# Kernel optimization log

Measured on AMD Instinct MI355X. Metric: run time of the kernel, lower is better.

## Reference

```python
import jax, jax.numpy as jnp
import numpy as np

B, S, D, H = 4, 2048, 1024, 16
DH = D // H
NEG = -10000.0


def setup_inputs() -> dict:
    key = jax.random.key(0)
    ks = jax.random.split(key, 12)
    scale = 0.02
    inp = {
        "q": jax.random.normal(ks[0], (B, S, D), jnp.float32),
        "k": jax.random.normal(ks[1], (B, S, D), jnp.float32),
        "v": jax.random.normal(ks[2], (B, S, D), jnp.float32),
        "mask": jnp.triu(jnp.ones((S, S), jnp.bool_), k=1),  # True = masked (causal)
        "Wq": jax.random.normal(ks[3], (D, D), jnp.float32) * scale,
        "bq": jnp.zeros((D,), jnp.float32),
        "Wk": jax.random.normal(ks[4], (D, D), jnp.float32) * scale,
        "bk": jnp.zeros((D,), jnp.float32),
        "Wv": jax.random.normal(ks[5], (D, D), jnp.float32) * scale,
        "bv": jnp.zeros((D,), jnp.float32),
        "Wo": jax.random.normal(ks[6], (D, D), jnp.float32) * scale,
        "bo": jnp.zeros((D,), jnp.float32),
    }
    return inp


def _split(x):
    # [B,S,D] -> [B,H,S,DH]
    return x.reshape(B, S, H, DH).transpose(0, 2, 1, 3)


def reference(q, k, v, mask, Wq, bq, Wk, bk, Wv, bv, Wo, bo):
    # torch Linear: y = x @ W.T + b
    qh = _split(q @ Wq.T + bq)
    kh = _split(k @ Wk.T + bk)
    vh = _split(v @ Wv.T + bv)
    # scaled dot-product scores: [B,H,S,S]
    scores = jnp.einsum("bhqd,bhkd->bhqk", qh, kh) / jnp.sqrt(jnp.float32(DH))
    scores = scores + jnp.where(mask, jnp.float32(NEG), jnp.float32(0.0))
    attn = jax.nn.softmax(scores, axis=-1)  # dropout_rate=0 -> identity
    out = jnp.einsum("bhqk,bhkd->bhqd", attn, vh)
    out = out.transpose(0, 2, 1, 3).reshape(B, S, D)
    return out @ Wo.T + bo
```

## Files before the change

kernel.cpp:

```cpp
#include <hip/hip_runtime.h>
#include <hip/hip_bf16.h>


#define B_ 4
#define S_ 2048
#define D_ 1024
#define H_ 16
#define DH_ 64
#define M_ (B_*S_)
#define MASKADD (-14427.0f)
#define QSCALE  (0.180336880f)

typedef __attribute__((ext_vector_type(8)))  __bf16 bf16x8;
typedef __attribute__((ext_vector_type(8)))  unsigned short ushort8;
typedef __attribute__((ext_vector_type(4)))  float f32x4;
typedef __attribute__((ext_vector_type(16))) float f32x16;

__device__ __forceinline__ unsigned short f2bf(float f) {
  __hip_bfloat16 h = __float2bfloat16(f);
  union { __hip_bfloat16 h; unsigned short u; } c; c.h = h; return c.u;
}

__device__ __forceinline__ f32x4 mfma16(bf16x8 a, bf16x8 b, f32x4 c) {
  return __builtin_amdgcn_mfma_f32_16x16x32_bf16(a, b, c, 0, 0, 0);
}
__device__ __forceinline__ f32x16 mfma32(bf16x8 a, bf16x8 b, f32x16 c) {
  return __builtin_amdgcn_mfma_f32_32x32x16_bf16(a, b, c, 0, 0, 0);
}

__device__ __forceinline__ unsigned cvtpk(float lo, float hi) {
  unsigned r;
  asm("v_cvt_pk_bf16_f32 %0, %1, %2" : "=v"(r) : "v"(lo), "v"(hi));
  return r;
}

__device__ __forceinline__ void gld_lds16(const void* g, void* l) {
  __builtin_amdgcn_global_load_lds(
      (const __attribute__((address_space(1))) unsigned int*)g,
      (__attribute__((address_space(3))) unsigned int*)l, 16, 0, 0);
}

__global__ void cvt4_kernel(const float* __restrict__ p0, const float* __restrict__ p1,
                            const float* __restrict__ p2, const float* __restrict__ p3,
                            unsigned short* __restrict__ o0, unsigned short* __restrict__ o1,
                            unsigned short* __restrict__ o2, unsigned short* __restrict__ o3,
                            int n4) {
  int i = blockIdx.x * blockDim.x + threadIdx.x;
  if (i >= n4) return;
  const float* in  = (blockIdx.y == 0) ? p0 : (blockIdx.y == 1 ? p1 : (blockIdx.y == 2 ? p2 : p3));
  unsigned short* out = (blockIdx.y == 0) ? o0 : (blockIdx.y == 1 ? o1 : (blockIdx.y == 2 ? o2 : o3));
  float4 f = reinterpret_cast<const float4*>(in)[i];
  ushort4 o;
  o.x = f2bf(f.x); o.y = f2bf(f.y); o.z = f2bf(f.z); o.w = f2bf(f.w);
  reinterpret_cast<ushort4*>(out)[i] = o;
}

template<bool F32A>
__device__ __forceinline__
void gemm_body(const void* __restrict__ Ap, const unsigned short* __restrict__ W,
               const float* __restrict__ bias, void* __restrict__ outp,
               int mode, bool sc,
               unsigned short* sA16, float* sA32, unsigned short* sB)
{
  const int tid  = threadIdx.x;
  const int lane = tid & 63, wid = tid >> 6;
  const int bx = blockIdx.x;
  const int j8 = bx & 7, i8 = bx >> 3;
  const int mt = j8*8 + (i8 >> 3), nt = i8 & 7;
  const int m0 = mt*128, n0 = nt*128;
  const int wr = wid >> 1, wc = wid & 1;
  const int g = lane >> 4;

  const float* A32 = (const float*)Ap;
  const unsigned short* A16 = (const unsigned short*)Ap;

  f32x4 acc[4][4];
  #pragma unroll
  for (int i = 0; i < 4; ++i)
    #pragma unroll
    for (int j = 0; j < 4; ++j)
      #pragma unroll
      for (int r = 0; r < 4; ++r) acc[i][j][r] = 0.0f;

  auto stageB = [&](int bufi, int kt) {
    const unsigned short* Wb = W + (size_t)n0*D_ + kt*32;
    #pragma unroll
    for (int p = 0; p < 2; ++p) {
      int r = 32*wid + 16*p + (lane >> 2);
      int c = (lane & 3) * 8;
      gld_lds16(Wb + (size_t)r*D_ + c, &sB[bufi*4096 + (32*wid + 16*p)*32]);
    }
  };
  auto stageA16 = [&](int bufi, int kt) {
    const unsigned short* Ab = A16 + (size_t)m0*D_ + kt*32;
    #pragma unroll
    for (int p = 0; p < 2; ++p) {
      int r = 32*wid + 16*p + (lane >> 2);
      int c = (lane & 3) * 8;
      gld_lds16(Ab + (size_t)r*D_ + c, &sA16[bufi*4096 + (32*wid + 16*p)*32]);
    }
  };
  auto stageA32 = [&](int bufi, int kt) {
    const float* Ab = A32 + (size_t)m0*D_ + kt*32;
    #pragma unroll
    for (int p = 0; p < 4; ++p) {
      int ch = 4*wid + p;
      int row = ch*8 + (lane >> 3);
      int cbs = ((lane & 7) * 16) ^ ((lane >> 3) << 4);
      gld_lds16(Ab + (size_t)row*D_ + (cbs >> 2), &sA32[bufi*4096 + ch*256]);
    }
  };

  if (F32A) stageA32(0, 0); else stageA16(0, 0);
  stageB(0, 0);

  const int NK = D_/32;
  int buf = 0;
  for (int kt = 0; kt < NK; ++kt) {
    __syncthreads();
    if (kt + 1 < NK) {
      if (F32A) stageA32(buf ^ 1, kt + 1);
      else      stageA16(buf ^ 1, kt + 1);
      stageB(buf ^ 1, kt + 1);
    }

    bf16x8 aF[4], bF[4];
    #pragma unroll
    for (int i = 0; i < 4; ++i) {
      int row = 64*wr + 16*i + (lane & 15);
      if (F32A) {
        const char* base = (const char*)(sA32 + buf*4096) + row*128;
        int sw = (row & 7) << 4;
        f32x4 a0 = *(const f32x4*)(base + ((g*32)      ^ sw));
        f32x4 a1 = *(const f32x4*)(base + ((g*32 + 16) ^ sw));
        union { unsigned u[4]; bf16x8 v; } af;
        af.u[0] = cvtpk(a0[0], a0[1]);
        af.u[1] = cvtpk(a0[2], a0[3]);
        af.u[2] = cvtpk(a1[0], a1[1]);
        af.u[3] = cvtpk(a1[2], a1[3]);
        aF[i] = af.v;
      } else {
        aF[i] = *(const bf16x8*)&sA16[buf*4096 + row*32 + g*8];
      }
    }
    #pragma unroll
    for (int j = 0; j < 4; ++j)
      bF[j] = *(const bf16x8*)&sB[buf*4096 + (64*wc + 16*j + (lane & 15))*32 + g*8];

    #pragma unroll
    for (int i = 0; i < 4; ++i)
      #pragma unroll
      for (int j = 0; j < 4; ++j)
        acc[i][j] = mfma16(aF[i], bF[j], acc[i][j]);
    buf ^= 1;
  }

  #pragma unroll
  for (int i = 0; i < 4; ++i) {
    int gr0 = m0 + 64*wr + 16*i + ((lane >> 4) << 2);
    #pragma unroll
    for (int j = 0; j < 4; ++j) {
      int gc = n0 + 64*wc + 16*j + (lane & 15);
      float bv = bias[gc];
      if (mode == 2) {
        int b = gr0 >> 11, s = gr0 & (S_ - 1);
        int hh = gc >> 6, dh = gc & (DH_ - 1);
        ushort4 o;
        o.x = f2bf(acc[i][j][0] + bv); o.y = f2bf(acc[i][j][1] + bv);
        o.z = f2bf(acc[i][j][2] + bv); o.w = f2bf(acc[i][j][3] + bv);
        *(ushort4*)&((unsigned short*)outp)[(((size_t)b*H_ + hh)*DH_ + dh)*S_ + s] = o;
      } else {
        #pragma unroll
        for (int r = 0; r < 4; ++r) {
          float v = acc[i][j][r] + bv;
          if (sc) v *= QSCALE;
          int gr = gr0 + r;
          if (mode == 0) {
            int b = gr >> 11, s = gr & (S_ - 1);
            int hh = gc >> 6, dh = gc & (DH_ - 1);
            ((unsigned short*)outp)[(((size_t)b*H_ + hh)*S_ + s)*DH_ + dh] = f2bf(v);
          } else {
            ((float*)outp)[(size_t)gr*D_ + gc] = v;
          }
        }
      }
    }
  }
}

__global__ __launch_bounds__(256, 3)
void gemm_qkv(const float* __restrict__ Aq, const float* __restrict__ Ak,
              const float* __restrict__ Av,
              const unsigned short* __restrict__ Wq_, const unsigned short* __restrict__ Wk_,
              const unsigned short* __restrict__ Wv_,
              const float* __restrict__ bq_, const float* __restrict__ bk_,
              const float* __restrict__ bv_,
              unsigned short* __restrict__ Oq, unsigned short* __restrict__ Ok,
              unsigned short* __restrict__ Ov)
{
  __shared__ float          sA32[2*4096];
  __shared__ unsigned short sB  [2*4096];
  const int y = blockIdx.y;
  const float* A = (y == 0) ? Aq : (y == 1 ? Ak : Av);
  const unsigned short* W = (y == 0) ? Wq_ : (y == 1 ? Wk_ : Wv_);
  const float* bias        = (y == 0) ? bq_ : (y == 1 ? bk_ : bv_);
  unsigned short* outp     = (y == 0) ? Oq  : (y == 1 ? Ok  : Ov);
  gemm_body<true>(A, W, bias, outp, (y == 2) ? 2 : 0, y == 0, nullptr, sA32, sB);
}

__global__ __launch_bounds__(256, 3)
void gemm_out(const unsigned short* __restrict__ A, const unsigned short* __restrict__ W,
              const float* __restrict__ bias, float* __restrict__ outp)
{
  __shared__ unsigned short sA16[2*4096];
  __shared__ unsigned short sB  [2*4096];
  gemm_body<false>(A, W, bias, outp, 1, false, sA16, nullptr, sB);
}

__global__ __launch_bounds__(256)
void attn_kernel(const unsigned short* __restrict__ Qh, const unsigned short* __restrict__ Kh,
                 const unsigned short* __restrict__ Vt, unsigned short* __restrict__ AO)
{
  __shared__ unsigned short sK [2][64*64];
  __shared__ unsigned short sVt[2][64*64];

  const int tid = threadIdx.x, lane = tid & 63, wid = tid >> 6;
  const int l31 = lane & 31, h5 = lane >> 5;
  const int bh = blockIdx.x;
  const int chunk = 15 - (int)blockIdx.y;
  const int bb = bh >> 4, hd = bh & 15;
  const unsigned short* Qb = Qh + (size_t)bh * S_ * DH_;
  const unsigned short* Kb = Kh + (size_t)bh * S_ * DH_;
  const unsigned short* Vb = Vt + (size_t)bh * DH_ * S_;
  const int qc0 = chunk * 128;
  const int NT  = 2*chunk + 2;
  const int qw0 = qc0 + wid*32;
  const int q   = qw0 + l31;

  bf16x8 qF[4];
  #pragma unroll
  for (int c = 0; c < 4; ++c)
    qF[c] = *(const bf16x8*)(Qb + (size_t)q*DH_ + c*16 + h5*8);

  f32x16 zz;
  #pragma unroll
  for (int r = 0; r < 16; ++r) zz[r] = 0.0f;
  f32x16 accO0 = zz, accO1 = zz;
  float lsum = 0.0f;

  auto stageK = [&](int bufi, int t) {
    #pragma unroll
    for (int p = 0; p < 2; ++p) {
      int ch = 2*wid + p;
      int row = ch*8 + (lane >> 3);
      int cbs = ((lane & 7) * 16) ^ ((row & 7) << 4);
      gld_lds16(Kb + (size_t)(t*64 + row)*DH_ + (cbs >> 1), &sK[bufi][ch*512]);
    }
  };
  auto stageV = [&](int bufi, int t) {
    #pragma unroll
    for (int p = 0; p < 2; ++p) {
      int ch = 2*wid + p;
      int row = ch*8 + (lane >> 3);
      int cbs = ((lane & 7) * 16) ^ ((row & 7) << 4);
      gld_lds16(Vb + (size_t)row*S_ + t*64 + (cbs >> 1), &sVt[bufi][ch*512]);
    }
  };

  stageK(0, 0);
  stageV(0, 0);

  int buf = 0;
  for (int t = 0; t < NT; ++t) {
    __syncthreads();
    if (t + 1 < NT) { stageK(buf ^ 1, t + 1); stageV(buf ^ 1, t + 1); }

    #pragma unroll
    for (int sub = 0; sub < 2; ++sub) {
      const int kv0 = t*64 + sub*32;
      if (kv0 > qw0 + 31) continue;
      const bool dodiag = (kv0 + 31 > qw0);

      f32x16 st = zz;
      __builtin_amdgcn_s_setprio(1);
      #pragma unroll
      for (int c = 0; c < 4; ++c) {
        int row = sub*32 + l31;
        const char* base = (const char*)&sK[buf][0] + row*128;
        bf16x8 kf = *(const bf16x8*)(base + ((32*c + 16*h5) ^ ((row & 7) << 4)));
        st = mfma32(kf, qF[c], st);
      }
      __builtin_amdgcn_s_setprio(0);

      #pragma unroll
      for (int r = 0; r < 16; ++r) {
        float x = st[r];
        if (dodiag) {
          int kv = kv0 + (r & 3) + 8*(r >> 2) + 4*h5;
          if (kv > q) x += MASKADD;
        }
        x = __builtin_amdgcn_exp2f(x);
        st[r] = x;
        lsum += x;
      }

      #pragma unroll
      for (int hh = 0; hh < 2; ++hh) {
        union { unsigned u[4]; bf16x8 v; } pb;
        pb.u[0] = cvtpk(st[8*hh+0], st[8*hh+1]);
        pb.u[1] = cvtpk(st[8*hh+2], st[8*hh+3]);
        pb.u[2] = cvtpk(st[8*hh+4], st[8*hh+5]);
        pb.u[3] = cvtpk(st[8*hh+6], st[8*hh+7]);

        __builtin_amdgcn_s_setprio(1);
        #pragma unroll
        for (int dh = 0; dh < 2; ++dh) {
          int row = dh*32 + l31;
          const char* base = (const char*)&sVt[buf][0] + row*128;
          int sw = (row & 7) << 4;
          int X = 64*sub + 32*hh + 8*h5;
          union { uint2 g[2]; bf16x8 v; } vv;
          vv.g[0] = *(const uint2*)(base + ((X)      ^ sw));
          vv.g[1] = *(const uint2*)(base + ((X + 16) ^ sw));
          if (dh == 0) accO0 = mfma32(vv.v, pb.v, accO0);
          else         accO1 = mfma32(vv.v, pb.v, accO1);
        }
        __builtin_amdgcn_s_setprio(0);
      }
    }
    buf ^= 1;
  }

  float lt = lsum + __shfl_xor(lsum, 32, 64);
  float inv = 1.0f / lt;
  unsigned short* ao = AO + ((size_t)bb*S_ + q)*D_ + hd*DH_;
  #pragma unroll
  for (int dh = 0; dh < 2; ++dh) {
    const f32x16 A = dh ? accO1 : accO0;
    #pragma unroll
    for (int rq = 0; rq < 4; ++rq) {
      ushort4 o;
      o.x = f2bf(A[4*rq+0] * inv);
      o.y = f2bf(A[4*rq+1] * inv);
      o.z = f2bf(A[4*rq+2] * inv);
      o.w = f2bf(A[4*rq+3] * inv);
      int dbase = dh*32 + 8*rq + 4*h5;
      *(ushort4*)&ao[dbase] = o;
    }
  }
}

extern "C" void kernel_launch(void* const* d_in, const int* in_sizes, int n_in,
                              void* d_out, int out_size, void* d_ws, size_t ws_size,
                              hipStream_t stream)
{
  const float* q  = (const float*)d_in[0];
  const float* k  = (const float*)d_in[1];
  const float* v  = (const float*)d_in[2];
  const float* Wq = (const float*)d_in[4];
  const float* bq = (const float*)d_in[5];
  const float* Wk = (const float*)d_in[6];
  const float* bk = (const float*)d_in[7];
  const float* Wv = (const float*)d_in[8];
  const float* bv = (const float*)d_in[9];
  const float* Wo = (const float*)d_in[10];
  const float* bo = (const float*)d_in[11];

  unsigned short* ws = (unsigned short*)d_ws;
  const size_t MD = (size_t)M_ * D_;
  const size_t DD = (size_t)D_ * D_;
  unsigned short* Wqb = ws;
  unsigned short* Wkb = Wqb + DD;
  unsigned short* Wvb = Wkb + DD;
  unsigned short* Wob = Wvb + DD;
  unsigned short* Qhb = Wob + DD;
  unsigned short* Khb = Qhb + MD;
  unsigned short* Vtb = Khb + MD;
  unsigned short* AOb = Vtb + MD;

  cvt4_kernel<<<dim3((int)(DD/4/256), 4), 256, 0, stream>>>(Wq, Wk, Wv, Wo, Wqb, Wkb, Wvb, Wob, (int)(DD/4));

  gemm_qkv<<<dim3(512, 3), 256, 0, stream>>>(q, k, v, Wqb, Wkb, Wvb,
                                             bq, bk, bv, Qhb, Khb, Vtb);

  attn_kernel<<<dim3(64, 16), 256, 0, stream>>>(Qhb, Khb, Vtb, AOb);

  gemm_out<<<512, 256, 0, stream>>>(AOb, Wob, bo, (float*)d_out);
}
```

Measured before the change: 175.8 us.

## Load fp32 activations directly to registers in QKV GEMM, bypassing LDS

The QKV projection GEMM no longer stages fp32 A tiles through shared memory. Each lane now loads its A fragment straight from global memory into registers, double-buffered across two register sets, and converts to bf16 just before the MFMA, while B stays staged in LDS. This removes the LDS traffic and the swizzled reads for A and cuts shared-memory use, at the cost of more registers (the occupancy hint of 3 is dropped) and less coalesced global reads of A. The out-projection GEMM is specialised inline and the shared epilogue is split into a helper.

```diff
diff --git a/kernel.cpp b/kernel.cpp
--- a/kernel.cpp
+++ b/kernel.cpp
@@ -55,106 +55,11 @@
   reinterpret_cast<ushort4*>(out)[i] = o;
 }
 
-template<bool F32A>
 __device__ __forceinline__
-void gemm_body(const void* __restrict__ Ap, const unsigned short* __restrict__ W,
-               const float* __restrict__ bias, void* __restrict__ outp,
-               int mode, bool sc,
-               unsigned short* sA16, float* sA32, unsigned short* sB)
+void gemm_epilogue(f32x4 (&acc)[4][4], const float* __restrict__ bias,
+                   void* __restrict__ outp, int mode, bool sc,
+                   int m0, int n0, int wr, int wc, int lane)
 {
-  const int tid  = threadIdx.x;
-  const int lane = tid & 63, wid = tid >> 6;
-  const int bx = blockIdx.x;
-  const int j8 = bx & 7, i8 = bx >> 3;
-  const int mt = j8*8 + (i8 >> 3), nt = i8 & 7;
-  const int m0 = mt*128, n0 = nt*128;
-  const int wr = wid >> 1, wc = wid & 1;
-  const int g = lane >> 4;
-
-  const float* A32 = (const float*)Ap;
-  const unsigned short* A16 = (const unsigned short*)Ap;
-
-  f32x4 acc[4][4];
-  #pragma unroll
-  for (int i = 0; i < 4; ++i)
-    #pragma unroll
-    for (int j = 0; j < 4; ++j)
-      #pragma unroll
-      for (int r = 0; r < 4; ++r) acc[i][j][r] = 0.0f;
-
-  auto stageB = [&](int bufi, int kt) {
-    const unsigned short* Wb = W + (size_t)n0*D_ + kt*32;
-    #pragma unroll
-    for (int p = 0; p < 2; ++p) {
-      int r = 32*wid + 16*p + (lane >> 2);
-      int c = (lane & 3) * 8;
-      gld_lds16(Wb + (size_t)r*D_ + c, &sB[bufi*4096 + (32*wid + 16*p)*32]);
-    }
-  };
-  auto stageA16 = [&](int bufi, int kt) {
-    const unsigned short* Ab = A16 + (size_t)m0*D_ + kt*32;
-    #pragma unroll
-    for (int p = 0; p < 2; ++p) {
-      int r = 32*wid + 16*p + (lane >> 2);
-      int c = (lane & 3) * 8;
-      gld_lds16(Ab + (size_t)r*D_ + c, &sA16[bufi*4096 + (32*wid + 16*p)*32]);
-    }
-  };
-  auto stageA32 = [&](int bufi, int kt) {
-    const float* Ab = A32 + (size_t)m0*D_ + kt*32;
-    #pragma unroll
-    for (int p = 0; p < 4; ++p) {
-      int ch = 4*wid + p;
-      int row = ch*8 + (lane >> 3);
-      int cbs = ((lane & 7) * 16) ^ ((lane >> 3) << 4);
-      gld_lds16(Ab + (size_t)row*D_ + (cbs >> 2), &sA32[bufi*4096 + ch*256]);
-    }
-  };
-
-  if (F32A) stageA32(0, 0); else stageA16(0, 0);
-  stageB(0, 0);
-
-  const int NK = D_/32;
-  int buf = 0;
-  for (int kt = 0; kt < NK; ++kt) {
-    __syncthreads();
-    if (kt + 1 < NK) {
-      if (F32A) stageA32(buf ^ 1, kt + 1);
-      else      stageA16(buf ^ 1, kt + 1);
-      stageB(buf ^ 1, kt + 1);
-    }
-
-    bf16x8 aF[4], bF[4];
-    #pragma unroll
-    for (int i = 0; i < 4; ++i) {
-      int row = 64*wr + 16*i + (lane & 15);
-      if (F32A) {
-        const char* base = (const char*)(sA32 + buf*4096) + row*128;
-        int sw = (row & 7) << 4;
-        f32x4 a0 = *(const f32x4*)(base + ((g*32)      ^ sw));
-        f32x4 a1 = *(const f32x4*)(base + ((g*32 + 16) ^ sw));
-        union { unsigned u[4]; bf16x8 v; } af;
-        af.u[0] = cvtpk(a0[0], a0[1]);
-        af.u[1] = cvtpk(a0[2], a0[3]);
-        af.u[2] = cvtpk(a1[0], a1[1]);
-        af.u[3] = cvtpk(a1[2], a1[3]);
-        aF[i] = af.v;
-      } else {
-        aF[i] = *(const bf16x8*)&sA16[buf*4096 + row*32 + g*8];
-      }
-    }
-    #pragma unroll
-    for (int j = 0; j < 4; ++j)
-      bF[j] = *(const bf16x8*)&sB[buf*4096 + (64*wc + 16*j + (lane & 15))*32 + g*8];
-
-    #pragma unroll
-    for (int i = 0; i < 4; ++i)
-      #pragma unroll
-      for (int j = 0; j < 4; ++j)
-        acc[i][j] = mfma16(aF[i], bF[j], acc[i][j]);
-    buf ^= 1;
-  }
-
   #pragma unroll
   for (int i = 0; i < 4; ++i) {
     int gr0 = m0 + 64*wr + 16*i + ((lane >> 4) << 2);
@@ -188,7 +93,7 @@
   }
 }
 
-__global__ __launch_bounds__(256, 3)
+__global__ __launch_bounds__(256)
 void gemm_qkv(const float* __restrict__ Aq, const float* __restrict__ Ak,
               const float* __restrict__ Av,
               const unsigned short* __restrict__ Wq_, const unsigned short* __restrict__ Wk_,
@@ -198,23 +103,158 @@
               unsigned short* __restrict__ Oq, unsigned short* __restrict__ Ok,
               unsigned short* __restrict__ Ov)
 {
-  __shared__ float          sA32[2*4096];
-  __shared__ unsigned short sB  [2*4096];
+  __shared__ unsigned short sB[2*4096];
   const int y = blockIdx.y;
   const float* A = (y == 0) ? Aq : (y == 1 ? Ak : Av);
   const unsigned short* W = (y == 0) ? Wq_ : (y == 1 ? Wk_ : Wv_);
   const float* bias        = (y == 0) ? bq_ : (y == 1 ? bk_ : bv_);
   unsigned short* outp     = (y == 0) ? Oq  : (y == 1 ? Ok  : Ov);
-  gemm_body<true>(A, W, bias, outp, (y == 2) ? 2 : 0, y == 0, nullptr, sA32, sB);
+  const int mode = (y == 2) ? 2 : 0;
+  const bool sc = (y == 0);
+
+  const int tid  = threadIdx.x;
+  const int lane = tid & 63, wid = tid >> 6;
+  const int bx = blockIdx.x;
+  const int j8 = bx & 7, i8 = bx >> 3;
+  const int mt = j8*8 + (i8 >> 3), nt = i8 & 7;
+  const int m0 = mt*128, n0 = nt*128;
+  const int wr = wid >> 1, wc = wid & 1;
+  const int g = lane >> 4;
+
+  f32x4 acc[4][4];
+  #pragma unroll
+  for (int i = 0; i < 4; ++i)
+    #pragma unroll
+    for (int j = 0; j < 4; ++j)
+      #pragma unroll
+      for (int r = 0; r < 4; ++r) acc[i][j][r] = 0.0f;
+
+  auto stageB = [&](int bufi, int kt) {
+    const unsigned short* Wb = W + (size_t)n0*D_ + kt*32;
+    #pragma unroll
+    for (int p = 0; p < 2; ++p) {
+      int r = 32*wid + 16*p + (lane >> 2);
+      int c = (lane & 3) * 8;
+      gld_lds16(Wb + (size_t)r*D_ + c, &sB[bufi*4096 + (32*wid + 16*p)*32]);
+    }
+  };
+
+  const float* arow[4];
+  #pragma unroll
+  for (int i = 0; i < 4; ++i)
+    arow[i] = A + (size_t)(m0 + 64*wr + 16*i + (lane & 15))*D_ + g*8;
+
+  f32x4 aR0[4][2], aR1[4][2];
+  auto loadA = [&](int kt, f32x4 (*aR)[2]) {
+    #pragma unroll
+    for (int i = 0; i < 4; ++i) {
+      const float* p = arow[i] + kt*32;
+      aR[i][0] = *(const f32x4*)(p);
+      aR[i][1] = *(const f32x4*)(p + 4);
+    }
+  };
+  auto mfmaStep = [&](const f32x4 (*aR)[2], int bufi) {
+    bf16x8 aF[4], bF[4];
+    #pragma unroll
+    for (int i = 0; i < 4; ++i) {
+      union { unsigned u[4]; bf16x8 v; } af;
+      af.u[0] = cvtpk(aR[i][0][0], aR[i][0][1]);
+      af.u[1] = cvtpk(aR[i][0][2], aR[i][0][3]);
+      af.u[2] = cvtpk(aR[i][1][0], aR[i][1][1]);
+      af.u[3] = cvtpk(aR[i][1][2], aR[i][1][3]);
+      aF[i] = af.v;
+    }
+    #pragma unroll
+    for (int j = 0; j < 4; ++j)
+      bF[j] = *(const bf16x8*)&sB[bufi*4096 + (64*wc + 16*j + (lane & 15))*32 + g*8];
+    #pragma unroll
+    for (int i = 0; i < 4; ++i)
+      #pragma unroll
+      for (int j = 0; j < 4; ++j)
+        acc[i][j] = mfma16(aF[i], bF[j], acc[i][j]);
+  };
+
+  loadA(0, aR0);
+  stageB(0, 0);
+
+  const int NK = D_/32;
+  for (int it = 0; it < NK/2; ++it) {
+    const int kt0 = 2*it;
+
+    __syncthreads();
+    stageB(1, kt0 + 1);
+    loadA(kt0 + 1, aR1);
+    mfmaStep(aR0, 0);
+
+    __syncthreads();
+    if (kt0 + 2 < NK) {
+      stageB(0, kt0 + 2);
+      loadA(kt0 + 2, aR0);
+    }
+    mfmaStep(aR1, 1);
+  }
+
+  gemm_epilogue(acc, bias, outp, mode, sc, m0, n0, wr, wc, lane);
 }
 
 __global__ __launch_bounds__(256, 3)
 void gemm_out(const unsigned short* __restrict__ A, const unsigned short* __restrict__ W,
               const float* __restrict__ bias, float* __restrict__ outp)
 {
-  __shared__ unsigned short sA16[2*4096];
-  __shared__ unsigned short sB  [2*4096];
-  gemm_body<false>(A, W, bias, outp, 1, false, sA16, nullptr, sB);
+  __shared__ unsigned short sA[2*4096];
+  __shared__ unsigned short sB[2*4096];
+
+  const int tid  = threadIdx.x;
+  const int lane = tid & 63, wid = tid >> 6;
+  const int bx = blockIdx.x;
+  const int j8 = bx & 7, i8 = bx >> 3;
+  const int mt = j8*8 + (i8 >> 3), nt = i8 & 7;
+  const int m0 = mt*128, n0 = nt*128;
+  const int wr = wid >> 1, wc = wid & 1;
+  const int g = lane >> 4;
+
+  f32x4 acc[4][4];
+  #pragma unroll
+  for (int i = 0; i < 4; ++i)
+    #pragma unroll
+    for (int j = 0; j < 4; ++j)
+      #pragma unroll
+      for (int r = 0; r < 4; ++r) acc[i][j][r] = 0.0f;
+
+  auto stage = [&](int bufi, int kt) {
+    const unsigned short* Ab = A + (size_t)m0*D_ + kt*32;
+    const unsigned short* Wb = W + (size_t)n0*D_ + kt*32;
+    #pragma unroll
+    for (int p = 0; p < 2; ++p) {
+      int r = 32*wid + 16*p + (lane >> 2);
+      int c = (lane & 3) * 8;
+      gld_lds16(Ab + (size_t)r*D_ + c, &sA[bufi*4096 + (32*wid + 16*p)*32]);
+      gld_lds16(Wb + (size_t)r*D_ + c, &sB[bufi*4096 + (32*wid + 16*p)*32]);
+    }
+  };
+
+  stage(0, 0);
+  const int NK = D_/32;
+  int buf = 0;
+  for (int kt = 0; kt < NK; ++kt) {
+    __syncthreads();
+    if (kt + 1 < NK) stage(buf ^ 1, kt + 1);
+    bf16x8 aF[4], bF[4];
+    #pragma unroll
+    for (int i = 0; i < 4; ++i)
+      aF[i] = *(const bf16x8*)&sA[buf*4096 + (64*wr + 16*i + (lane & 15))*32 + g*8];
+    #pragma unroll
+    for (int j = 0; j < 4; ++j)
+      bF[j] = *(const bf16x8*)&sB[buf*4096 + (64*wc + 16*j + (lane & 15))*32 + g*8];
+    #pragma unroll
+    for (int i = 0; i < 4; ++i)
+      #pragma unroll
+      for (int j = 0; j < 4; ++j)
+        acc[i][j] = mfma16(aF[i], bF[j], acc[i][j]);
+    buf ^= 1;
+  }
+
+  gemm_epilogue(acc, bias, outp, 1, false, m0, n0, wr, wc, lane);
 }
 
 __global__ __launch_bounds__(256)
```

Result: slower. 298.6 us (+69.8%).
